# Kernel tuning notes

Measured on AMD Instinct MI355X. Metric: run time of the kernel, lower is better.

## Reference

```python
import jax, jax.numpy as jnp
import numpy as np

N_EMBD = 1024
N_HEAD = 16
B, L = 4, 2048


def setup_inputs() -> dict:
    key = jax.random.key(0)
    ks = jax.random.split(key, 5)
    scale = 1.0 / np.sqrt(N_EMBD)
    x = jax.random.normal(ks[0], (B, L, N_EMBD), dtype=jnp.float32)
    # nn.Linear(n_embd, n_embd, bias=False) weights, stored torch-style (out, in)
    Wq = jax.random.uniform(ks[1], (N_EMBD, N_EMBD), jnp.float32, -scale, scale)
    Wk = jax.random.uniform(ks[2], (N_EMBD, N_EMBD), jnp.float32, -scale, scale)
    Wv = jax.random.uniform(ks[3], (N_EMBD, N_EMBD), jnp.float32, -scale, scale)
    Wp = jax.random.uniform(ks[4], (N_EMBD, N_EMBD), jnp.float32, -scale, scale)
    attn_mask = jnp.ones((B, L), dtype=jnp.int32)
    return {"x": x, "Wq": Wq, "Wk": Wk, "Wv": Wv, "Wp": Wp, "attn_mask": attn_mask}


def reference(x, Wq, Wk, Wv, Wp, attn_mask):
    Bq, Lq, C = x.shape
    hd = C // N_HEAD
    # torch Linear: y = x @ W.T
    def split_heads(y):
        return y.reshape(Bq, Lq, N_HEAD, hd).transpose(0, 2, 1, 3)  # (B,H,L,hd)
    q = split_heads(x @ Wq.T)
    k = split_heads(x @ Wk.T)
    v = split_heads(x @ Wv.T)
    att = jnp.einsum("bhqd,bhkd->bhqk", q, k) / np.sqrt(hd)  # (B,H,L,L)
    causal = jnp.tril(jnp.ones((Lq, Lq), dtype=bool))
    neg_inf = jnp.float32(-jnp.inf)
    att = jnp.where(causal[None, None, :, :], att, neg_inf)
    pad = (attn_mask != 0)[:, None, None, :]  # (B,1,1,L) key-side padding mask
    att = jnp.where(pad, att, neg_inf)
    att = jax.nn.softmax(att, axis=-1)
    y = jnp.einsum("bhqk,bhkd->bhqd", att, v)
    y = y.transpose(0, 2, 1, 3).reshape(Bq, Lq, C)
    return y @ Wp.T
```

## Files before the change

### kernel.cpp

```cpp
#include <hip/hip_runtime.h>

typedef __attribute__((ext_vector_type(8))) short short8;
typedef __attribute__((ext_vector_type(4))) float floatx4;

#define CEMB 1024
#define NHEAD 16
#define HD 64
#define BATCH 4
#define SEQ 2048

#define BARRIER() asm volatile("s_waitcnt lgkmcnt(0)\n\ts_barrier" ::: "memory")

__device__ __forceinline__ unsigned short f2bf(float f) {
    union { float f; unsigned int i; } x; x.f = f;
    unsigned int r = x.i + 0x7FFFu + ((x.i >> 16) & 1u);
    return (unsigned short)(r >> 16);
}
__device__ __forceinline__ unsigned int packbf_trunc(float a, float b) {
    union { float f; unsigned int u; } x, y; x.f = a; y.f = b;
    return (x.u >> 16) | (y.u & 0xFFFF0000u);
}

#define GLD16(gp, lp) \
    __builtin_amdgcn_global_load_lds((const __attribute__((address_space(1))) void*)(gp), \
                                     (__attribute__((address_space(3))) void*)(lp), 16, 0, 0)

__global__ void cast_x(const float* __restrict__ src, unsigned short* __restrict__ dst, int n4) {
    int i = blockIdx.x * blockDim.x + threadIdx.x;
    if (i < n4) {
        float4 v = ((const float4*)src)[i];
        ushort4 o;
        o.x = f2bf(v.x); o.y = f2bf(v.y); o.z = f2bf(v.z); o.w = f2bf(v.w);
        ((ushort4*)dst)[i] = o;
    }
}

__global__ void cast_w(const float* __restrict__ w0, const float* __restrict__ w1,
                       const float* __restrict__ w2, const float* __restrict__ w3,
                       unsigned short* __restrict__ o0, unsigned short* __restrict__ o1,
                       unsigned short* __restrict__ o2, unsigned short* __restrict__ o3) {
    int which = blockIdx.y;
    const float* src = which == 0 ? w0 : which == 1 ? w1 : which == 2 ? w2 : w3;
    unsigned short* dst = which == 0 ? o0 : which == 1 ? o1 : which == 2 ? o2 : o3;
    float scale = (which == 0) ? 0.125f * 1.44269504088896f : 1.0f;
    int i = blockIdx.x * blockDim.x + threadIdx.x;
    float4 v = ((const float4*)src)[i];
    ushort4 o;
    o.x = f2bf(v.x * scale); o.y = f2bf(v.y * scale);
    o.z = f2bf(v.z * scale); o.w = f2bf(v.w * scale);
    ((ushort4*)dst)[i] = o;
}


#define MFMA __builtin_amdgcn_mfma_f32_16x16x32_bf16

#define PH(Ab, Bb, mh, nh) do {                                                 \
    short8 af[4][2], bfr[2][2];                                                 \
    _Pragma("unroll")                                                           \
    for (int mm = 0; mm < 4; ++mm) {                                            \
        af[mm][0] = *(const short8*)((Ab) + aOffR + (mh)*4096 + mm*1024 + ck0); \
        af[mm][1] = *(const short8*)((Ab) + aOffR + (mh)*4096 + mm*1024 + ck1); \
    }                                                                           \
    _Pragma("unroll")                                                           \
    for (int nn = 0; nn < 2; ++nn) {                                            \
        bfr[nn][0] = *(const short8*)((Bb) + bOffR + (nh)*2048 + nn*1024 + ck0);\
        bfr[nn][1] = *(const short8*)((Bb) + bOffR + (nh)*2048 + nn*1024 + ck1);\
    }                                                                           \
    __builtin_amdgcn_s_setprio(1);                                              \
    _Pragma("unroll")                                                           \
    for (int mm = 0; mm < 4; ++mm)                                              \
        _Pragma("unroll")                                                       \
        for (int nn = 0; nn < 2; ++nn) {                                        \
            acc[(mh)*4+mm][(nh)*2+nn] = MFMA(af[mm][0], bfr[nn][0],             \
                                             acc[(mh)*4+mm][(nh)*2+nn], 0,0,0); \
            acc[(mh)*4+mm][(nh)*2+nn] = MFMA(af[mm][1], bfr[nn][1],             \
                                             acc[(mh)*4+mm][(nh)*2+nn], 0,0,0); \
        }                                                                       \
    __builtin_amdgcn_s_setprio(0);                                              \
    __builtin_amdgcn_sched_barrier(0);                                          \
} while (0)

#define STAGE(Ab, Bb, k0) do {                                                  \
    GLD16(aS + (k0),             (Ab) + aLA);                                   \
    GLD16(aS + (k0) +  8 * CEMB, (Ab) + aLA + 512);                             \
    GLD16(bS + (k0),             (Bb) + aLB);                                   \
    GLD16(bS + (k0) +  8 * CEMB, (Bb) + aLB + 512);                             \
    GLD16(bS + (k0) + 16 * CEMB, (Bb) + aLB + 1024);                            \
    GLD16(bS + (k0) + 24 * CEMB, (Bb) + aLB + 1536);                            \
} while (0)

#define PH4(Ab, Bb, t, do_stage) do {                                           \
    short8 af[4][2], bfr[2][2];                                                 \
    _Pragma("unroll")                                                           \
    for (int mm = 0; mm < 4; ++mm) {                                            \
        af[mm][0] = *(const short8*)((Ab) + aOffR + mm*1024 + ck0);             \
        af[mm][1] = *(const short8*)((Ab) + aOffR + mm*1024 + ck1);             \
    }                                                                           \
    _Pragma("unroll")                                                           \
    for (int nn = 0; nn < 2; ++nn) {                                            \
        bfr[nn][0] = *(const short8*)((Bb) + bOffR + 2048 + nn*1024 + ck0);     \
        bfr[nn][1] = *(const short8*)((Bb) + bOffR + 2048 + nn*1024 + ck1);     \
    }                                                                           \
    asm volatile("s_waitcnt lgkmcnt(0)\n\ts_barrier" ::: "memory");             \
    __builtin_amdgcn_sched_barrier(0);                                          \
    if (do_stage) STAGE(Ab, Bb, ((t) + 2) * 64);                                \
    __builtin_amdgcn_s_setprio(1);                                              \
    _Pragma("unroll")                                                           \
    for (int mm = 0; mm < 4; ++mm)                                              \
        _Pragma("unroll")                                                       \
        for (int nn = 0; nn < 2; ++nn) {                                        \
            acc[mm][2+nn] = MFMA(af[mm][0], bfr[nn][0], acc[mm][2+nn], 0,0,0);  \
            acc[mm][2+nn] = MFMA(af[mm][1], bfr[nn][1], acc[mm][2+nn], 0,0,0);  \
        }                                                                       \
    __builtin_amdgcn_s_setprio(0);                                              \
    __builtin_amdgcn_sched_barrier(0);                                          \
} while (0)

#define TILE(t, drain, do_stage) do {                                           \
    unsigned short* Ab = &As[(t) & 1][0];                                       \
    unsigned short* Bb = &Bs[(t) & 1][0];                                       \
    if (drain) { asm volatile("s_waitcnt vmcnt(0)" ::: "memory"); }             \
    else       { asm volatile("s_waitcnt vmcnt(6)" ::: "memory"); }             \
    asm volatile("s_barrier" ::: "memory");                                     \
    PH(Ab, Bb, 0, 0);                                                           \
    PH4(Ab, Bb, t, do_stage);                                                   \
} while (0)

__launch_bounds__(512, 2)
__global__ void gemm_128(const unsigned short* __restrict__ A,
                         const unsigned short* __restrict__ W,
                         void* __restrict__ O0, void* __restrict__ O1,
                         void* __restrict__ O2, int mode, int ntn) {
    __shared__ unsigned short As[2][8192];
    __shared__ unsigned short Bs[2][16384];

    int nwg = gridDim.x;
    int bid = blockIdx.x;
    int wg = (bid & 7) * (nwg >> 3) + (bid >> 3);
    int cpr = ntn >> 2;
    int c = wg >> 5, r = wg & 31;
    int cm = c / cpr, cn = c - cm * cpr;
    int mt = cm * 8 + (r >> 2);
    int nt = cn * 4 + (r & 3);
    int m0 = mt * 128, n0 = nt * 256;

    int tid = threadIdx.x;
    int wave = tid >> 6, lane = tid & 63;
    int l16 = lane & 15, quad = lane >> 4;
    int wm = wave >> 2, wn = wave & 3;

    int srow = lane >> 3;
    int scol = ((lane & 7) ^ srow) * 8;
    const unsigned short* aS = A + (size_t)(m0 + wave * 16 + srow) * CEMB + scol;
    const unsigned short* bS = W + (size_t)(n0 + wave * 32 + srow) * CEMB + scol;
    int aLA = wave * 1024;
    int aLB = wave * 2048;

    int aOffR = (wm * 64 + l16) * 64;
    int bOffR = (wn * 64 + l16) * 64;
    int ck0 = (quad ^ (l16 & 7)) * 8;
    int ck1 = ck0 ^ 32;

    floatx4 acc[4][4];
    #pragma unroll
    for (int mm = 0; mm < 4; ++mm)
        #pragma unroll
        for (int nn = 0; nn < 4; ++nn) acc[mm][nn] = (floatx4){0.f, 0.f, 0.f, 0.f};

    STAGE(&As[0][0], &Bs[0][0], 0);
    STAGE(&As[1][0], &Bs[1][0], 64);

    #pragma unroll 2
    for (int t = 0; t < 14; ++t) { TILE(t, false, true); }
    TILE(14, false, false);
    TILE(15, true, false);

    if (mode == 1) {
        float* Of = (float*)O0;
        #pragma unroll
        for (int mf = 0; mf < 4; ++mf)
            #pragma unroll
            for (int j = 0; j < 4; ++j) {
                int m = m0 + wm * 64 + mf * 16 + quad * 4 + j;
                #pragma unroll
                for (int nf = 0; nf < 4; ++nf) {
                    int n = n0 + wn * 64 + nf * 16 + l16;
                    Of[(size_t)m * CEMB + n] = acc[mf][nf][j];
                }
            }
    } else {
        int which = n0 >> 10;
        unsigned short* out = (unsigned short*)(which == 0 ? O0 : which == 1 ? O1 : O2);
        if (which < 2) {
            #pragma unroll
            for (int mf = 0; mf < 4; ++mf)
                #pragma unroll
                for (int j = 0; j < 4; ++j) {
                    int m = m0 + wm * 64 + mf * 16 + quad * 4 + j;
                    int bb = m >> 11, ll = m & (SEQ - 1);
                    #pragma unroll
                    for (int nf = 0; nf < 4; ++nf) {
                        int n = (n0 & (CEMB - 1)) + wn * 64 + nf * 16 + l16;
                        int h = n >> 6, d = n & (HD - 1);
                        out[(size_t)((bb * NHEAD + h) * SEQ + ll) * HD + d] =
                            f2bf(acc[mf][nf][j]);
                    }
                }
        } else {
            #pragma unroll
            for (int mf = 0; mf < 4; ++mf) {
                int m = m0 + wm * 64 + mf * 16 + quad * 4;
                int bb = m >> 11, ll = m & (SEQ - 1);
                #pragma unroll
                for (int nf = 0; nf < 4; ++nf) {
                    int n = (n0 & (CEMB - 1)) + wn * 64 + nf * 16 + l16;
                    int h = n >> 6, d = n & (HD - 1);
                    ushort4 o4;
                    o4.x = f2bf(acc[mf][nf][0]); o4.y = f2bf(acc[mf][nf][1]);
                    o4.z = f2bf(acc[mf][nf][2]); o4.w = f2bf(acc[mf][nf][3]);
                    *(ushort4*)&out[(size_t)((bb * NHEAD + h) * HD + d) * SEQ + ll] = o4;
                }
            }
        }
    }
}

__launch_bounds__(256, 2)
__global__ void attn_mfma(const unsigned short* __restrict__ Qb,
                          const unsigned short* __restrict__ Kb,
                          const unsigned short* __restrict__ Vtg,
                          const int* __restrict__ amask,
                          unsigned short* __restrict__ Yb) {
    __shared__ unsigned short Ks[64 * 64];
    __shared__ unsigned short Vs[64 * 64];
    __shared__ unsigned short Ps[128 * 64];

    int tid = threadIdx.x;
    int wave = tid >> 6;
    int lane = tid & 63;
    int l16 = lane & 15;
    int quad = lane >> 4;
    int l7 = l16 & 7;

    int n = blockIdx.x;
    int rr = n >> 8;
    int i = n & 255;
    int base = i & 15;
    int bh = (i >> 4) + (rr << 4);
    int qt = (rr == 0) ? base
           : (rr == 1) ? 15 - base
           : (rr == 2) ? (base ^ 8)
                       : 15 - (base ^ 8);

    int bidx = bh >> 4;
    int h = bh & (NHEAD - 1);
    size_t hbase = (size_t)bh * SEQ * HD;

    int r0 = tid >> 3, p0 = tid & 7;
    int cl = p0 ^ (r0 & 7);
    unsigned short* kDst0 = Ks + r0 * 64 + p0 * 8;
    unsigned short* kDst1 = kDst0 + 32 * 64;
    unsigned short* vDst0 = Vs + r0 * 64 + p0 * 8;
    unsigned short* vDst1 = vDst0 + 32 * 64;
    const unsigned short* kSrc0 = Kb + hbase + (size_t)r0 * HD + cl * 8;
    const unsigned short* kSrc1 = kSrc0 + (size_t)32 * HD;
    const unsigned short* vSrc0 = Vtg + hbase + (size_t)r0 * SEQ + cl * 8;
    const unsigned short* vSrc1 = vSrc0 + (size_t)32 * SEQ;
    const int* mSrc = amask + bidx * SEQ + quad * 4;

    int q0 = qt * 128;
    int nkt = 2 * qt + 2;

    short8 qf[2][2];
    #pragma unroll
    for (int qsub = 0; qsub < 2; ++qsub)
        #pragma unroll
        for (int kk = 0; kk < 2; ++kk)
            qf[qsub][kk] = *(const short8*)(Qb + hbase +
                (size_t)(q0 + wave * 32 + qsub * 16 + l16) * HD + kk * 32 + quad * 8);

    short8 kr0 = *(const short8*)(kSrc0);
    short8 kr1 = *(const short8*)(kSrc1);
    short8 vr0 = *(const short8*)(vSrc0);
    short8 vr1 = *(const short8*)(vSrc1);
    int4 cmi[4];
    #pragma unroll
    for (int t = 0; t < 4; ++t) cmi[t] = *(const int4*)(mSrc + t * 16);

    floatx4 o[2][4];
    #pragma unroll
    for (int qsub = 0; qsub < 2; ++qsub)
        #pragma unroll
        for (int t = 0; t < 4; ++t) o[qsub][t] = (floatx4){0.f, 0.f, 0.f, 0.f};
    float ls[2] = {0.f, 0.f};

    int qw = q0 + wave * 32;

    for (int jt = 0; jt < nkt; ++jt) {
        BARRIER();
        *(short8*)kDst0 = kr0;
        *(short8*)kDst1 = kr1;
        *(short8*)vDst0 = vr0;
        *(short8*)vDst1 = vr1;
        int4 cm[4];
        #pragma unroll
        for (int t = 0; t < 4; ++t) cm[t] = cmi[t];
        if (jt + 1 < nkt) {
            size_t ko = (size_t)(jt + 1) * 64;
            kr0 = *(const short8*)(kSrc0 + ko * HD);
            kr1 = *(const short8*)(kSrc1 + ko * HD);
            vr0 = *(const short8*)(vSrc0 + ko);
            vr1 = *(const short8*)(vSrc1 + ko);
            #pragma unroll
            for (int t = 0; t < 4; ++t) cmi[t] = *(const int4*)(mSrc + (jt + 1) * 64 + t * 16);
        }
        BARRIER();

        if (jt * 64 <= qw + 31) {
            floatx4 sc[2][4];
            #pragma unroll
            for (int qsub = 0; qsub < 2; ++qsub)
                #pragma unroll
                for (int t = 0; t < 4; ++t) sc[qsub][t] = (floatx4){0.f, 0.f, 0.f, 0.f};
            #pragma unroll
            for (int kk = 0; kk < 2; ++kk)
                #pragma unroll
                for (int t = 0; t < 4; ++t) {
                    short8 aK = *(const short8*)(Ks + (t * 16 + l16) * 64 +
                                                 ((kk * 4 + quad) ^ l7) * 8);
                    #pragma unroll
                    for (int qsub = 0; qsub < 2; ++qsub)
                        sc[qsub][t] = __builtin_amdgcn_mfma_f32_16x16x32_bf16(
                            aK, qf[qsub][kk], sc[qsub][t], 0, 0, 0);
                }

            bool needc = (jt * 64 + 63 > qw);

            #pragma unroll
            for (int qsub = 0; qsub < 2; ++qsub) {
                int qi = q0 + wave * 32 + qsub * 16 + l16;
                #pragma unroll
                for (int t = 0; t < 4; ++t) {
                    int kb = jt * 64 + t * 16 + quad * 4;
                    float p[4];
                    #pragma unroll
                    for (int j = 0; j < 4; ++j) {
                        float sv = sc[qsub][t][j];
                        if (needc) sv = (kb + j <= qi) ? sv : -1e30f;
                        sv = cm[t][j] ? sv : -1e30f;
                        p[j] = __builtin_amdgcn_exp2f(sv);
                        ls[qsub] += p[j];
                    }
                    int row = wave * 32 + qsub * 16 + l16;
                    int pos = (t * 2 + (quad >> 1)) ^ l7;
                    uint2 pk;
                    pk.x = packbf_trunc(p[0], p[1]);
                    pk.y = packbf_trunc(p[2], p[3]);
                    *(uint2*)(Ps + row * 64 + pos * 8 + (quad & 1) * 4) = pk;
                }
            }

            #pragma unroll
            for (int kk = 0; kk < 2; ++kk) {
                short8 pa[2];
                #pragma unroll
                for (int qsub = 0; qsub < 2; ++qsub)
                    pa[qsub] = *(const short8*)(Ps + (wave * 32 + qsub * 16 + l16) * 64 +
                                                ((kk * 4 + quad) ^ l7) * 8);
                #pragma unroll
                for (int t = 0; t < 4; ++t) {
                    short8 vb = *(const short8*)(Vs + (t * 16 + l16) * 64 +
                                                 ((kk * 4 + quad) ^ l7) * 8);
                    #pragma unroll
                    for (int qsub = 0; qsub < 2; ++qsub)
                        o[qsub][t] = __builtin_amdgcn_mfma_f32_16x16x32_bf16(
                            pa[qsub], vb, o[qsub][t], 0, 0, 0);
                }
            }
        }
    }

    #pragma unroll
    for (int qsub = 0; qsub < 2; ++qsub) {
        ls[qsub] += __shfl_xor(ls[qsub], 16, 64);
        ls[qsub] += __shfl_xor(ls[qsub], 32, 64);
    }

    #pragma unroll
    for (int qsub = 0; qsub < 2; ++qsub)
        #pragma unroll
        for (int j = 0; j < 4; ++j) {
            float lq = __shfl(ls[qsub], quad * 4 + j, 64);
            float inv = 1.0f / lq;
            size_t row = (size_t)bidx * SEQ + q0 + wave * 32 + qsub * 16 + quad * 4 + j;
            #pragma unroll
            for (int t = 0; t < 4; ++t)
                Yb[row * CEMB + h * HD + t * 16 + l16] = f2bf(o[qsub][t][j] * inv);
        }
}

extern "C" void kernel_launch(void* const* d_in, const int* in_sizes, int n_in,
                              void* d_out, int out_size, void* d_ws, size_t ws_size,
                              hipStream_t stream) {
    const float* x  = (const float*)d_in[0];
    const float* Wq = (const float*)d_in[1];
    const float* Wk = (const float*)d_in[2];
    const float* Wv = (const float*)d_in[3];
    const float* Wp = (const float*)d_in[4];
    const int* amask = (const int*)d_in[5];

    char* ws = (char*)d_ws;
    unsigned short* xb  = (unsigned short*)(ws + 0);
    unsigned short* Wqb = (unsigned short*)(ws + (16u << 20));
    unsigned short* Wkb = (unsigned short*)(ws + (18u << 20));
    unsigned short* Wvb = (unsigned short*)(ws + (20u << 20));
    unsigned short* Wpb = (unsigned short*)(ws + (22u << 20));
    unsigned short* Qb  = (unsigned short*)(ws + (24u << 20));
    unsigned short* Kb  = (unsigned short*)(ws + (40u << 20));
    unsigned short* Vtg = (unsigned short*)(ws + (56u << 20));
    unsigned short* Yb  = (unsigned short*)(ws + (72u << 20));

    const int NX4 = (BATCH * SEQ * CEMB) / 4;
    const int NW4 = (CEMB * CEMB) / 4;
    cast_x<<<dim3(NX4 / 256), 256, 0, stream>>>(x, xb, NX4);
    cast_w<<<dim3(NW4 / 256, 4), 256, 0, stream>>>(Wq, Wk, Wv, Wp, Wqb, Wkb, Wvb, Wpb);

    gemm_128<<<dim3(768), 512, 0, stream>>>(
        xb, Wqb, (void*)Qb, (void*)Kb, (void*)Vtg, 0, 12);

    attn_mfma<<<dim3(1024), 256, 0, stream>>>(Qb, Kb, Vtg, amask, Yb);

    gemm_128<<<dim3(256), 512, 0, stream>>>(
        Yb, Wpb, d_out, nullptr, nullptr, 1, 4);
}
```

Measured before the change: 256.0 us.

## Shrink GEMM tile to 128x128 with 4 waves and double the grid

```diff
diff --git a/kernel.cpp b/kernel.cpp
--- a/kernel.cpp
+++ b/kernel.cpp
@@ -54,39 +54,39 @@
 
 #define MFMA __builtin_amdgcn_mfma_f32_16x16x32_bf16
 
-#define PH(Ab, Bb, mh, nh) do {                                                 \
+#define PH(Ab, Bb) do {                                                         \
     short8 af[4][2], bfr[2][2];                                                 \
     _Pragma("unroll")                                                           \
     for (int mm = 0; mm < 4; ++mm) {                                            \
-        af[mm][0] = *(const short8*)((Ab) + aOffR + (mh)*4096 + mm*1024 + ck0); \
-        af[mm][1] = *(const short8*)((Ab) + aOffR + (mh)*4096 + mm*1024 + ck1); \
+        af[mm][0] = *(const short8*)((Ab) + aOffR + mm*1024 + ck0);             \
+        af[mm][1] = *(const short8*)((Ab) + aOffR + mm*1024 + ck1);             \
     }                                                                           \
     _Pragma("unroll")                                                           \
     for (int nn = 0; nn < 2; ++nn) {                                            \
-        bfr[nn][0] = *(const short8*)((Bb) + bOffR + (nh)*2048 + nn*1024 + ck0);\
-        bfr[nn][1] = *(const short8*)((Bb) + bOffR + (nh)*2048 + nn*1024 + ck1);\
+        bfr[nn][0] = *(const short8*)((Bb) + bOffR + nn*1024 + ck0);            \
+        bfr[nn][1] = *(const short8*)((Bb) + bOffR + nn*1024 + ck1);            \
     }                                                                           \
     __builtin_amdgcn_s_setprio(1);                                              \
     _Pragma("unroll")                                                           \
     for (int mm = 0; mm < 4; ++mm)                                              \
         _Pragma("unroll")                                                       \
         for (int nn = 0; nn < 2; ++nn) {                                        \
-            acc[(mh)*4+mm][(nh)*2+nn] = MFMA(af[mm][0], bfr[nn][0],             \
-                                             acc[(mh)*4+mm][(nh)*2+nn], 0,0,0); \
-            acc[(mh)*4+mm][(nh)*2+nn] = MFMA(af[mm][1], bfr[nn][1],             \
-                                             acc[(mh)*4+mm][(nh)*2+nn], 0,0,0); \
+            acc[mm][nn] = MFMA(af[mm][0], bfr[nn][0], acc[mm][nn], 0,0,0);      \
+            acc[mm][nn] = MFMA(af[mm][1], bfr[nn][1], acc[mm][nn], 0,0,0);      \
         }                                                                       \
     __builtin_amdgcn_s_setprio(0);                                              \
     __builtin_amdgcn_sched_barrier(0);                                          \
 } while (0)
 
 #define STAGE(Ab, Bb, k0) do {                                                  \
-    GLD16(aS + (k0),             (Ab) + aLA);                                   \
-    GLD16(aS + (k0) +  8 * CEMB, (Ab) + aLA + 512);                             \
-    GLD16(bS + (k0),             (Bb) + aLB);                                   \
-    GLD16(bS + (k0) +  8 * CEMB, (Bb) + aLB + 512);                             \
-    GLD16(bS + (k0) + 16 * CEMB, (Bb) + aLB + 1024);                            \
-    GLD16(bS + (k0) + 24 * CEMB, (Bb) + aLB + 1536);                            \
+    GLD16(aS + (k0),             (Ab) + aLS);                                   \
+    GLD16(aS + (k0) +  8 * CEMB, (Ab) + aLS + 512);                             \
+    GLD16(aS + (k0) + 16 * CEMB, (Ab) + aLS + 1024);                            \
+    GLD16(aS + (k0) + 24 * CEMB, (Ab) + aLS + 1536);                            \
+    GLD16(bS + (k0),             (Bb) + aLS);                                   \
+    GLD16(bS + (k0) +  8 * CEMB, (Bb) + aLS + 512);                             \
+    GLD16(bS + (k0) + 16 * CEMB, (Bb) + aLS + 1024);                            \
+    GLD16(bS + (k0) + 24 * CEMB, (Bb) + aLS + 1536);                            \
 } while (0)
 
 #define PH4(Ab, Bb, t, do_stage) do {                                           \
@@ -98,8 +98,8 @@
     }                                                                           \
     _Pragma("unroll")                                                           \
     for (int nn = 0; nn < 2; ++nn) {                                            \
-        bfr[nn][0] = *(const short8*)((Bb) + bOffR + 2048 + nn*1024 + ck0);     \
-        bfr[nn][1] = *(const short8*)((Bb) + bOffR + 2048 + nn*1024 + ck1);     \
+        bfr[nn][0] = *(const short8*)((Bb) + bOffR + (2+nn)*1024 + ck0);        \
+        bfr[nn][1] = *(const short8*)((Bb) + bOffR + (2+nn)*1024 + ck1);        \
     }                                                                           \
     asm volatile("s_waitcnt lgkmcnt(0)\n\ts_barrier" ::: "memory");             \
     __builtin_amdgcn_sched_barrier(0);                                          \
@@ -120,19 +120,19 @@
     unsigned short* Ab = &As[(t) & 1][0];                                       \
     unsigned short* Bb = &Bs[(t) & 1][0];                                       \
     if (drain) { asm volatile("s_waitcnt vmcnt(0)" ::: "memory"); }             \
-    else       { asm volatile("s_waitcnt vmcnt(6)" ::: "memory"); }             \
+    else       { asm volatile("s_waitcnt vmcnt(8)" ::: "memory"); }             \
     asm volatile("s_barrier" ::: "memory");                                     \
-    PH(Ab, Bb, 0, 0);                                                           \
+    PH(Ab, Bb);                                                                 \
     PH4(Ab, Bb, t, do_stage);                                                   \
 } while (0)
 
-__launch_bounds__(512, 2)
+__launch_bounds__(256, 2)
 __global__ void gemm_128(const unsigned short* __restrict__ A,
                          const unsigned short* __restrict__ W,
                          void* __restrict__ O0, void* __restrict__ O1,
                          void* __restrict__ O2, int mode, int ntn) {
     __shared__ unsigned short As[2][8192];
-    __shared__ unsigned short Bs[2][16384];
+    __shared__ unsigned short Bs[2][8192];
 
     int nwg = gridDim.x;
     int bid = blockIdx.x;
@@ -142,19 +142,18 @@
     int cm = c / cpr, cn = c - cm * cpr;
     int mt = cm * 8 + (r >> 2);
     int nt = cn * 4 + (r & 3);
-    int m0 = mt * 128, n0 = nt * 256;
+    int m0 = mt * 128, n0 = nt * 128;
 
     int tid = threadIdx.x;
     int wave = tid >> 6, lane = tid & 63;
     int l16 = lane & 15, quad = lane >> 4;
-    int wm = wave >> 2, wn = wave & 3;
+    int wm = wave >> 1, wn = wave & 1;
 
     int srow = lane >> 3;
     int scol = ((lane & 7) ^ srow) * 8;
-    const unsigned short* aS = A + (size_t)(m0 + wave * 16 + srow) * CEMB + scol;
+    const unsigned short* aS = A + (size_t)(m0 + wave * 32 + srow) * CEMB + scol;
     const unsigned short* bS = W + (size_t)(n0 + wave * 32 + srow) * CEMB + scol;
-    int aLA = wave * 1024;
-    int aLB = wave * 2048;
+    int aLS = wave * 2048;
 
     int aOffR = (wm * 64 + l16) * 64;
     int bOffR = (wn * 64 + l16) * 64;
@@ -425,11 +424,11 @@
     cast_x<<<dim3(NX4 / 256), 256, 0, stream>>>(x, xb, NX4);
     cast_w<<<dim3(NW4 / 256, 4), 256, 0, stream>>>(Wq, Wk, Wv, Wp, Wqb, Wkb, Wvb, Wpb);
 
-    gemm_128<<<dim3(768), 512, 0, stream>>>(
-        xb, Wqb, (void*)Qb, (void*)Kb, (void*)Vtg, 0, 12);
+    gemm_128<<<dim3(1536), 256, 0, stream>>>(
+        xb, Wqb, (void*)Qb, (void*)Kb, (void*)Vtg, 0, 24);
 
     attn_mfma<<<dim3(1024), 256, 0, stream>>>(Qb, Kb, Vtg, amask, Yb);
 
-    gemm_128<<<dim3(256), 512, 0, stream>>>(
-        Yb, Wpb, d_out, nullptr, nullptr, 1, 4);
-}
+    gemm_128<<<dim3(512), 256, 0, stream>>>(
+        Yb, Wpb, d_out, nullptr, nullptr, 1, 8);
+}
```

After: 247.3 us. 3.4% less time.
